# Performance work log

Measured on AMD Instinct MI355X. Metric: run time of the kernel, lower is better.

The kernel has to match this reference:

```python
import jax, jax.numpy as jnp
import numpy as np

B, P, N, E, F, L = 64, 512, 512, 128, 512, 6
SQRT_E = 11.313708498984761
CLIP = 10.0
EPS = 1e-5

def _inorm(x, w, b):
    # InstanceNorm1d over node dim (axis=1) per (batch, channel); x: [B,N,E]
    mu = x.mean(axis=1, keepdims=True)
    var = x.var(axis=1, keepdims=True)
    return (x - mu) * jax.lax.rsqrt(var + EPS) * w + b

def setup_inputs():
    key = jax.random.key(0)
    ks = jax.random.split(key, 24)
    nrm = lambda k, shp, s=0.05: jax.random.normal(k, shp, dtype=jnp.float32) * s
    inp = {}
    inp['data'] = jax.random.uniform(ks[0], (B, N, 2), dtype=jnp.float32)
    inp['dist'] = -jax.random.uniform(ks[1], (B, N, N), dtype=jnp.float32)      # negative dist
    inp['cur_dist'] = -jax.random.uniform(ks[2], (B, P, N), dtype=jnp.float32)
    inp['capacity'] = jax.random.uniform(ks[3], (B, P), dtype=jnp.float32)
    inp['ninf_mask'] = jnp.zeros((B, P, N), jnp.float32)
    inp['log_scale'] = jnp.array([1.0], jnp.float32)
    # encoder params (Linear weights stored [in,out], i.e. torch weight transposed)
    inp['emb_W'] = nrm(ks[4], (2, E), 0.5); inp['emb_b'] = jnp.zeros((E,), jnp.float32)
    inp['Wq'] = nrm(ks[5], (L, E, E)); inp['Wk'] = nrm(ks[6], (L, E, E)); inp['Wv'] = nrm(ks[7], (L, E, E))
    inp['aft_alpha'] = jnp.ones((L,), jnp.float32)
    inp['n1_w'] = jnp.ones((L, E), jnp.float32); inp['n1_b'] = jnp.zeros((L, E), jnp.float32)
    inp['ff_W1'] = nrm(ks[8], (L, E, F)); inp['ff_b1'] = jnp.zeros((L, F), jnp.float32)
    inp['ff_W2'] = nrm(ks[9], (L, F, E)); inp['ff_b2'] = jnp.zeros((L, E), jnp.float32)
    inp['n2_w'] = jnp.ones((L, E), jnp.float32); inp['n2_b'] = jnp.zeros((L, E), jnp.float32)
    # decoder params
    inp['dWq'] = nrm(ks[10], (E + 1, E)); inp['dWk'] = nrm(ks[11], (E, E)); inp['dWv'] = nrm(ks[12], (E, E))
    inp['dec_aft_alpha'] = jnp.array([1.0], jnp.float32)
    inp['probs_alpha'] = jnp.array([1.0], jnp.float32)
    return inp

def reference(data, dist, cur_dist, capacity, ninf_mask, log_scale,
              emb_W, emb_b, Wq, Wk, Wv, aft_alpha, n1_w, n1_b,
              ff_W1, ff_b1, ff_W2, ff_b2, n2_w, n2_b,
              dWq, dWk, dWv, dec_aft_alpha, probs_alpha):
    ls = log_scale[0]
    # ---- encoder: stacked AFT layers ----
    x = data @ emb_W + emb_b                                   # [B,N,E]
    for l in range(L):
        q = x @ Wq[l]; k = x @ Wk[l]; v = x @ Wv[l]
        ad = jnp.exp(ls * aft_alpha[l] * dist)                 # [B,N,N]
        ek = jnp.exp(k)
        weighted = (ad @ (ek * v)) / (ad @ ek)                 # [B,N,E]
        out = jax.nn.sigmoid(q) * weighted
        h = _inorm(x + out, n1_w[l], n1_b[l])
        ff = jax.nn.relu(h @ ff_W1[l] + ff_b1[l]) @ ff_W2[l] + ff_b2[l]
        x = _inorm(h + ff, n2_w[l], n2_b[l])
    enc = x                                                    # [B,N,E]
    # ---- decoder ----
    k = enc @ dWk; v = enc @ dWv
    gmean = enc.mean(axis=1, keepdims=True)                    # [B,1,E]
    gmp = jnp.broadcast_to(gmean, (enc.shape[0], capacity.shape[1], enc.shape[2]))
    q = jnp.concatenate([gmp, capacity[:, :, None]], axis=2) @ dWq   # [B,P,E]
    ad = jnp.exp(ls * dec_aft_alpha[0] * cur_dist + ninf_mask)       # [B,P,N]
    ek = jnp.exp(k)
    weighted = (ad @ (ek * v)) / (ad @ ek)                     # [B,P,E]
    aft = jax.nn.sigmoid(q) * weighted
    score = jnp.einsum('bpe,bne->bpn', aft, enc) / SQRT_E
    score = score + ls * probs_alpha[0] * cur_dist
    score = CLIP * jnp.tanh(score) + ninf_mask
    return jax.nn.softmax(score, axis=2)                       # [B,P,N]
```

## Files before the change

kernel.cpp:

```cpp
#include <hip/hip_runtime.h>
#include <math.h>

#define B_ 64
#define N_ 512
#define P_ 512
#define E_ 128
#define F_ 512
#define L_ 6
#define SQRT_E_INV 0.08838834764831843f

typedef unsigned short u16;
typedef __attribute__((ext_vector_type(8))) short bf8;
typedef __attribute__((ext_vector_type(16))) float f16v;

__device__ inline u16 bf16r(float f) {
    unsigned u = __float_as_uint(f);
    u += 0x7fffu + ((u >> 16) & 1u);
    return (u16)(u >> 16);
}
__device__ inline float bf2f(u16 h) { return __uint_as_float((unsigned)h << 16); }

#define MFMA(a, b, c) __builtin_amdgcn_mfma_f32_32x32x16_bf16(a, b, c, 0, 0, 0)

struct Q3 {
    const u16 *A0, *A1;
    const u16 *qh, *ql, *vh, *vl, *kh, *kl;
    u16 *sq16, *y2t;
};

__launch_bounds__(256, 2) __global__ void qvk3_k(Q3 p)
{
    const int tid = threadIdx.x;
    const int lane = tid & 63, wv = tid >> 6;
    const int wm = wv & 1, wn = wv >> 1;
    const int ln = lane & 31, hk = lane >> 5;
    const int row0 = blockIdx.x * 64;

    __shared__ __align__(16) u16 As[2][64][40];
    __shared__ __align__(16) u16 Bs[6][128][40];

    f16v aq[2], av[2], ak[2];
#pragma unroll
    for (int nt = 0; nt < 2; ++nt)
#pragma unroll
        for (int q = 0; q < 16; ++q) { aq[nt][q] = 0.f; av[nt][q] = 0.f; ak[nt][q] = 0.f; }

    const int r = tid >> 2, kq = tid & 3;
    for (int k0 = 0; k0 < 128; k0 += 32) {
        size_t ga = (size_t)(row0 + r) * 128 + k0 + kq * 8;
        *(uint4*)&As[0][r][kq * 8] = *(const uint4*)(p.A0 + ga);
        *(uint4*)&As[1][r][kq * 8] = *(const uint4*)(p.A1 + ga);
#pragma unroll
        for (int i = 0; i < 2; ++i) {
            int s = tid + i * 256;
            int rb2 = s >> 2, q = s & 3;
            size_t gb = (size_t)rb2 * 128 + k0 + q * 8;
            *(uint4*)&Bs[0][rb2][q * 8] = *(const uint4*)(p.qh + gb);
            *(uint4*)&Bs[1][rb2][q * 8] = *(const uint4*)(p.ql + gb);
            *(uint4*)&Bs[2][rb2][q * 8] = *(const uint4*)(p.vh + gb);
            *(uint4*)&Bs[3][rb2][q * 8] = *(const uint4*)(p.vl + gb);
            *(uint4*)&Bs[4][rb2][q * 8] = *(const uint4*)(p.kh + gb);
            *(uint4*)&Bs[5][rb2][q * 8] = *(const uint4*)(p.kl + gb);
        }
        __syncthreads();
#pragma unroll
        for (int s = 0; s < 2; ++s) {
            bf8 ah = *(const bf8*)&As[0][wm * 32 + ln][s * 16 + hk * 8];
            bf8 al = *(const bf8*)&As[1][wm * 32 + ln][s * 16 + hk * 8];
#pragma unroll
            for (int nt = 0; nt < 2; ++nt) {
                const int br = wn * 64 + nt * 32 + ln, sc = s * 16 + hk * 8;
                bf8 bqh = *(const bf8*)&Bs[0][br][sc];
                bf8 bql = *(const bf8*)&Bs[1][br][sc];
                bf8 bvh = *(const bf8*)&Bs[2][br][sc];
                bf8 bvl = *(const bf8*)&Bs[3][br][sc];
                bf8 bkh = *(const bf8*)&Bs[4][br][sc];
                bf8 bkl = *(const bf8*)&Bs[5][br][sc];
                aq[nt] = MFMA(ah, bqh, aq[nt]);
                aq[nt] = MFMA(ah, bql, aq[nt]);
                aq[nt] = MFMA(al, bqh, aq[nt]);
                av[nt] = MFMA(ah, bvh, av[nt]);
                av[nt] = MFMA(ah, bvl, av[nt]);
                av[nt] = MFMA(al, bvh, av[nt]);
                ak[nt] = MFMA(ah, bkh, ak[nt]);
// ... 5 lines not shown
    }

#pragma unroll
    for (int nt = 0; nt < 2; ++nt) {
        int gn = wn * 64 + nt * 32 + ln;
#pragma unroll
        for (int g = 0; g < 4; ++g) {
            int rb = row0 + wm * 32 + g * 8 + hk * 4;
            int bb = rb >> 9, nb = rb & 511;
            u16 pe[4], pv[4];
#pragma unroll
            for (int rr = 0; rr < 4; ++rr) {
                float vq = aq[nt][g * 4 + rr];
                p.sq16[(size_t)(rb + rr) * 128 + gn] =
                    bf16r(1.f / (1.f + __expf(-vq)));
                u16 hv = bf16r(av[nt][g * 4 + rr]);
                u16 he = bf16r(__expf(ak[nt][g * 4 + rr]));
                pe[rr] = he;
                pv[rr] = bf16r(bf2f(hv) * bf2f(he));
            }
            uint2 ue, uv;
            ue.x = pe[0] | ((unsigned)pe[1] << 16);
            ue.y = pe[2] | ((unsigned)pe[3] << 16);
            uv.x = pv[0] | ((unsigned)pv[1] << 16);
            uv.y = pv[2] | ((unsigned)pv[3] << 16);
            *(uint2*)(p.y2t + (size_t)bb * 131072 + (size_t)gn * 512 + nb) = uv;
            *(uint2*)(p.y2t + (size_t)bb * 131072 + (size_t)(128 + gn) * 512 + nb) = ue;
        }
    }
}

struct QV {
    const u16 *A0, *A1;
    const u16 *vh, *vl, *kh, *kl;
    u16* y2t;
};

__launch_bounds__(256, 3) __global__ void qvk_vk_k(QV p)
{
    const int tid = threadIdx.x;
    const int lane = tid & 63, wv = tid >> 6;
    const int wm = wv & 1, wn = wv >> 1;
    const int ln = lane & 31, hk = lane >> 5;
    const int row0 = blockIdx.x * 64;

    __shared__ __align__(16) u16 As[2][64][40];
    __shared__ __align__(16) u16 Bs[4][128][40];

    f16v av[2], ak[2];
#pragma unroll
    for (int nt = 0; nt < 2; ++nt)
#pragma unroll
        for (int q = 0; q < 16; ++q) { av[nt][q] = 0.f; ak[nt][q] = 0.f; }

    const int r = tid >> 2, kq = tid & 3;
    for (int k0 = 0; k0 < 128; k0 += 32) {
        size_t ga = (size_t)(row0 + r) * 128 + k0 + kq * 8;
        *(uint4*)&As[0][r][kq * 8] = *(const uint4*)(p.A0 + ga);
        *(uint4*)&As[1][r][kq * 8] = *(const uint4*)(p.A1 + ga);
#pragma unroll
        for (int i = 0; i < 2; ++i) {
            int s = tid + i * 256;
            int rb2 = s >> 2, q = s & 3;
            size_t gb = (size_t)rb2 * 128 + k0 + q * 8;
            *(uint4*)&Bs[0][rb2][q * 8] = *(const uint4*)(p.vh + gb);
            *(uint4*)&Bs[1][rb2][q * 8] = *(const uint4*)(p.vl + gb);
            *(uint4*)&Bs[2][rb2][q * 8] = *(const uint4*)(p.kh + gb);
            *(uint4*)&Bs[3][rb2][q * 8] = *(const uint4*)(p.kl + gb);
        }
        __syncthreads();
#pragma unroll
        for (int s = 0; s < 2; ++s) {
            bf8 ah = *(const bf8*)&As[0][wm * 32 + ln][s * 16 + hk * 8];
            bf8 al = *(const bf8*)&As[1][wm * 32 + ln][s * 16 + hk * 8];
#pragma unroll
            for (int nt = 0; nt < 2; ++nt) {
                const int br = wn * 64 + nt * 32 + ln, sc = s * 16 + hk * 8;
                bf8 bvh = *(const bf8*)&Bs[0][br][sc];
                bf8 bvl = *(const bf8*)&Bs[1][br][sc];
                bf8 bkh = *(const bf8*)&Bs[2][br][sc];
                bf8 bkl = *(const bf8*)&Bs[3][br][sc];
                av[nt] = MFMA(ah, bvh, av[nt]);
                av[nt] = MFMA(ah, bvl, av[nt]);
                av[nt] = MFMA(al, bvh, av[nt]);
                ak[nt] = MFMA(ah, bkh, ak[nt]);
                ak[nt] = MFMA(ah, bkl, ak[nt]);
                ak[nt] = MFMA(al, bkh, ak[nt]);
            }
        }
        __syncthreads();
    }

#pragma unroll
    for (int nt = 0; nt < 2; ++nt) {
        int gn = wn * 64 + nt * 32 + ln;
#pragma unroll
        for (int g = 0; g < 4; ++g) {
            int rb = row0 + wm * 32 + g * 8 + hk * 4;
            int bb = rb >> 9, nb = rb & 511;
            u16 pe[4], pv[4];
#pragma unroll
            for (int rr = 0; rr < 4; ++rr) {
                u16 hv = bf16r(av[nt][g * 4 + rr]);
                u16 he = bf16r(__expf(ak[nt][g * 4 + rr]));
                pe[rr] = he;
                pv[rr] = bf16r(bf2f(hv) * bf2f(he));
            }
            uint2 ue, uv;
            ue.x = pe[0] | ((unsigned)pe[1] << 16);
            ue.y = pe[2] | ((unsigned)pe[3] << 16);
            uv.x = pv[0] | ((unsigned)pv[1] << 16);
            uv.y = pv[2] | ((unsigned)pv[3] << 16);
            *(uint2*)(p.y2t + (size_t)bb * 131072 + (size_t)gn * 512 + nb) = uv;
            *(uint2*)(p.y2t + (size_t)bb * 131072 + (size_t)(128 + gn) * 512 + nb) = ue;
        }
    }
}

struct AP2 {
    const u16 *A16;
    const u16 *B0, *sq;
    u16 *gh, *gl;
    const float *s1, *s2; int s2i;
    const float *gq, *cap, *dWq;
};

template <int OPA, int SG>
__launch_bounds__(256, 3) __global__ void aft2_k(AP2 p)
{
    const int tid = threadIdx.x;
    const int lane = tid & 63, wv = tid >> 6;
    const int wm = wv & 1, wn = wv >> 1;
    const int ln = lane & 31, hk = lane >> 5;

    const int id = blockIdx.x;
    const int xcd = id & 7, slot = id >> 3;
    const int bz = xcd * 8 + (slot >> 3);
    const int row0 = (slot & 7) * 64;

    __shared__ __align__(16) u16 As[2][64][40];
    __shared__ __align__(16) u16 Bs[2][256][40];

    f16v acc[4];
#pragma unroll
    for (int j = 0; j < 4; ++j)
#pragma unroll
        for (int q = 0; q < 16; ++q) acc[j][q] = 0.f;

    const float ascale = (OPA == 1) ? p.s1[0] * p.s2[p.s2i] : 0.f;
    const u16* Af = p.A16 + (size_t)bz * 262144 + (size_t)row0 * 512;
    const u16* Bb = p.B0 + (size_t)bz * 131072;

    const int r = tid >> 2, kq = tid & 3;
    uint4 va;
    uint4 vb[4];

#define AFT_LOAD(K0)                                                          \
    {                                                                         \
        va = *(const uint4*)(Af + (size_t)r * 512 + (K0) + kq * 8);           \
        size_t gb = (size_t)tid * 512 + (K0);                                 \
// ... 21 lines not shown
            *(uint4*)&Bs[BUF][tid][q * 8] = vb[q];                            \
    }

#define AFT_COMPUTE(BUF)                                                      \
    {                                                                         \
        _Pragma("unroll") for (int s = 0; s < 2; ++s) {                       \
            bf8 ah = *(const bf8*)&As[BUF][wm * 32 + ln][s * 16 + hk * 8];    \
            _Pragma("unroll") for (int j = 0; j < 4; ++j) {                   \
                int br = ((j >> 1) << 7) + wn * 64 + ((j & 1) << 5) + ln;     \
                bf8 bh = *(const bf8*)&Bs[BUF][br][s * 16 + hk * 8];          \
                acc[j] = MFMA(ah, bh, acc[j]);                                \
            }                                                                 \
        }                                                                     \
    }

    AFT_LOAD(0);
    AFT_WRITE(0);
    __syncthreads();

    int cur = 0;
    for (int k0 = 32; k0 < 512; k0 += 32) {
        AFT_LOAD(k0);
        AFT_COMPUTE(cur);
        AFT_WRITE(cur ^ 1);
        __syncthreads();
        cur ^= 1;
    }
    AFT_COMPUTE(cur);

#undef AFT_LOAD
#undef AFT_WRITE
#undef AFT_COMPUTE

    const u16* sqb = (SG == 1) ? (p.sq + (size_t)bz * 65536) : (const u16*)0;
    u16* ghb = p.gh + (size_t)bz * 65536;
    u16* glb = p.gl + (size_t)bz * 65536;
#pragma unroll
    for (int j = 0; j < 2; ++j) {
        int e = wn * 64 + j * 32 + ln;
#pragma unroll
        for (int g = 0; g < 4; ++g) {
#pragma unroll
            for (int rr = 0; rr < 4; ++rr) {
                int row = row0 + wm * 32 + g * 8 + hk * 4 + rr;
                float num = acc[j][g * 4 + rr];
                float den = acc[j + 2][g * 4 + rr];
                float pv = num / den;
                if (SG == 1) pv *= bf2f(sqb[(size_t)row * 128 + e]);
                if (SG == 2) {
                    float qv = fmaf(p.cap[(size_t)bz * 512 + row],
                                    p.dWq[128 * 128 + e], p.gq[bz * 128 + e]);
                    pv *= 1.f / (1.f + __expf(-qv));
                }
                u16 hi = bf16r(pv);
                ghb[(size_t)row * 128 + e] = hi;
                glb[(size_t)row * 128 + e] = bf16r(pv - bf2f(hi));
            }
        }
    }
}

struct F12 {
    const u16 *A0, *A1;
    const u16 *w1h, *w1l;
    const u16 *w2h, *w2l;
    const float *b1, *b2;
    float* of;
};

__launch_bounds__(512, 2) __global__ void ffn12_k(F12 p)
{
    const int tid = threadIdx.x;
    const int lane = tid & 63, wv = tid >> 6;
    const int wm = wv & 1, wn = wv >> 1;
    const int ln = lane & 31, hk = lane >> 5;
    const int row0 = blockIdx.x * 64;

    __shared__ __align__(16) u16 Ws[2][2][128][72];
    __shared__ __align__(16) u16 ff1c[4][64][136];

    bf8 ar0[8], ar1[8];
    {
        const size_t arow = (size_t)(row0 + wm * 32 + ln) * 128;
#pragma unroll
        for (int s = 0; s < 8; ++s) {
            ar0[s] = *(const bf8*)(p.A0 + arow + s * 16 + hk * 8);
            ar1[s] = *(const bf8*)(p.A1 + arow + s * 16 + hk * 8);
        }
    }

    const int lcol = wn * 32 + ln;
    const int sc_ = tid >> 3, sq_ = tid & 7;
    uint4 wr[2][2];

#define F_LOAD1(CT, KC)                                                       \
    {                                                                         \
        _Pragma("unroll") for (int pl = 0; pl < 2; ++pl) {                    \
            const u16* src = pl ? p.w1l : p.w1h;                              \
            _Pragma("unroll") for (int it = 0; it < 2; ++it) {                \
                int c = sc_ + it * 64;                                        \
                wr[pl][it] = *(const uint4*)(src +                            \
                    (size_t)((CT) * 128 + c) * 128 + (KC) * 64 + sq_ * 8);    \
            }                                                                 \
        }                                                                     \
    }

#define F_LOAD2(J)                                                            \
    {                                                                         \
        _Pragma("unroll") for (int pl = 0; pl < 2; ++pl) {                    \
            const u16* src = pl ? p.w2l : p.w2h;                              \
            _Pragma("unroll") for (int it = 0; it < 2; ++it) {                \
                int c = sc_ + it * 64;                                        \
                wr[pl][it] = *(const uint4*)(src +                            \
                    (size_t)c * 512 + (J) * 64 + sq_ * 8);                    \
            }                                                                 \
        }                                                                     \
    }

#define F_STORE(BUF)                                                          \
    {                                                                         \
// ... 36 lines not shown
                }
        }
        F_STORE(buf ^ 1);
        __syncthreads();
        buf ^= 1;
    }

    f16v c0, c1;
#pragma unroll
    for (int q = 0; q < 16; ++q) { c0[q] = 0.f; c1[q] = 0.f; }
#pragma unroll
    for (int j = 0; j < 8; ++j) {
        if (j < 7) F_LOAD2(j + 1);
#pragma unroll
        for (int s = 0; s < 4; ++s) {
            bf8 af = *(const bf8*)&ff1c[j >> 1][wm * 32 + ln]
                                      [(j & 1) * 64 + s * 16 + hk * 8];
            bf8 bh = *(const bf8*)&Ws[buf][0][lcol][s * 16 + hk * 8];
            bf8 bl = *(const bf8*)&Ws[buf][1][lcol][s * 16 + hk * 8];
            c0 = MFMA(af, bh, c0);
            c1 = MFMA(af, bl, c1);
        }
        if (j < 7) {
            F_STORE(buf ^ 1);
            __syncthreads();
            buf ^= 1;
        }
    }

#undef F_LOAD1
#undef F_LOAD2
#undef F_STORE

    float bv = p.b2[lcol];
#pragma unroll
    for (int g = 0; g < 4; ++g)
#pragma unroll
        for (int rr = 0; rr < 4; ++rr) {
            int rb = row0 + wm * 32 + g * 8 + hk * 4 + rr;
            p.of[(size_t)rb * 128 + lcol] = c0[g * 4 + rr] + c1[g * 4 + rr] + bv;
        }
}

struct SP2 {
    const u16 *A0, *A1, *B0, *B1;
    float* out;
    const float *cd, *cm;
    const float *s1, *s2;
};

__launch_bounds__(1024, 4) __global__ void score_sm_k(SP2 p)
{
    const int tid = threadIdx.x;
    const int lane = tid & 63, wv = tid >> 6;
    const int wm = wv & 1, wn = wv >> 1;
    const int ln = lane & 31, hk = lane >> 5;

    const int id = blockIdx.x;
    const int xcd = id & 7, s_ = id >> 3;
    const int bz = xcd * 8 + (s_ & 7);
    const int row0 = (s_ >> 3) * 64;

    __shared__ __align__(16) u16 As[2][64][136];
    __shared__ __align__(16) u16 Bs[2][512][40];
    __shared__ float rs[8][64];

#pragma unroll
    for (int i = 0; i < 2; ++i) {
        int idx = tid + i * 1024;
        int pl = idx >> 10, rem = idx & 1023;
        int row = rem >> 4, q = rem & 15;
        const u16* src = pl ? p.A1 : p.A0;
        *(uint4*)&As[pl][row][q * 8] =
            *(const uint4*)(src + ((size_t)bz * 512 + row0 + row) * 128 + q * 8);
    }

    const float sp = p.s1[0] * p.s2[0];

    f16v accs[2];
#pragma unroll
    for (int nt = 0; nt < 2; ++nt)
#pragma unroll
        for (int q = 0; q < 16; ++q) accs[nt][q] = 0.f;

    for (int k0 = 0; k0 < 128; k0 += 32) {
#pragma unroll
        for (int i = 0; i < 4; ++i) {
            int idx = tid + i * 1024;
            int pl = idx >> 11, rem = idx & 2047;
            int row = rem >> 2, q = rem & 3;
            const u16* src = pl ? p.B1 : p.B0;
            *(uint4*)&Bs[pl][row][q * 8] =
                *(const uint4*)(src + ((size_t)bz * 512 + row) * 128 + k0 + q * 8);
        }
        __syncthreads();
#pragma unroll
        for (int s = 0; s < 2; ++s) {
            bf8 ah = *(const bf8*)&As[0][wm * 32 + ln][k0 + s * 16 + hk * 8];
            bf8 al = *(const bf8*)&As[1][wm * 32 + ln][k0 + s * 16 + hk * 8];
#pragma unroll
            for (int nt = 0; nt < 2; ++nt) {
                bf8 bh = *(const bf8*)&Bs[0][wn * 64 + nt * 32 + ln][s * 16 + hk * 8];
                bf8 bl = *(const bf8*)&Bs[1][wn * 64 + nt * 32 + ln][s * 16 + hk * 8];
                accs[nt] = MFMA(ah, bh, accs[nt]);
                accs[nt] = MFMA(ah, bl, accs[nt]);
                accs[nt] = MFMA(al, bh, accs[nt]);
            }
        }
        __syncthreads();
    }

    float rsum[16];
#pragma unroll
    for (int nt = 0; nt < 2; ++nt) {
        const int gn = wn * 64 + nt * 32 + ln;
        float cdv[16], cmv[16];
#pragma unroll
        for (int g = 0; g < 4; ++g)
#pragma unroll
            for (int rr = 0; rr < 4; ++rr) {
                int grow = row0 + wm * 32 + g * 8 + hk * 4 + rr;
                size_t ix = (size_t)bz * 262144 + (size_t)grow * 512 + gn;
                cdv[g * 4 + rr] = p.cd[ix];
                cmv[g * 4 + rr] = p.cm[ix];
            }
#pragma unroll
// ... 11 lines not shown
    for (int i = 0; i < 16; ++i) {
#pragma unroll
        for (int o = 1; o < 32; o <<= 1) rsum[i] += __shfl_xor(rsum[i], o);
    }
    __syncthreads();
    if (ln == 0) {
#pragma unroll
        for (int i = 0; i < 16; ++i) {
            int lr = wm * 32 + (i >> 2) * 8 + hk * 4 + (i & 3);
            rs[wn][lr] = rsum[i];
        }
    }
    __syncthreads();
    float invr[16];
#pragma unroll
    for (int i = 0; i < 16; ++i) {
        int lr = wm * 32 + (i >> 2) * 8 + hk * 4 + (i & 3);
        float t = rs[0][lr] + rs[1][lr] + rs[2][lr] + rs[3][lr]
                + rs[4][lr] + rs[5][lr] + rs[6][lr] + rs[7][lr];
        invr[i] = 1.f / t;
    }

#pragma unroll
    for (int nt = 0; nt < 2; ++nt) {
        int gn = wn * 64 + nt * 32 + ln;
#pragma unroll
        for (int g = 0; g < 4; ++g)
#pragma unroll
            for (int rr = 0; rr < 4; ++rr) {
                int grow = row0 + wm * 32 + g * 8 + hk * 4 + rr;
                size_t ix = (size_t)bz * 262144 + (size_t)grow * 512 + gn;
                p.out[ix] = accs[nt][g * 4 + rr] * invr[g * 4 + rr];
            }
    }
}

template <int MODE>
__launch_bounds__(256) __global__ void inorm_k(
    const u16* __restrict__ ah, const u16* __restrict__ al,
    const u16* __restrict__ g0, const u16* __restrict__ g1,
    const float* __restrict__ f1,
    const float* __restrict__ nw, const float* __restrict__ nbv,
    u16* __restrict__ oh, u16* __restrict__ ol)
{
    const int bb = blockIdx.x, e0 = blockIdx.y * 16;
    const int tid = threadIdx.x, el = tid & 3, no = tid >> 2;
    const size_t base = (size_t)bb * N_ * E_ + e0 + el * 4;

    float4 vals[8];
    float s1x = 0, s1y = 0, s1z = 0, s1w = 0;
    float s2x = 0, s2y = 0, s2z = 0, s2w = 0;
#pragma unroll
    for (int i = 0; i < 8; ++i) {
        int n = no * 8 + i;
        size_t ad = base + (size_t)n * E_;
        uint2 h2 = *(const uint2*)(ah + ad);
        uint2 l2 = *(const uint2*)(al + ad);
        float x0 = bf2f((u16)h2.x) + bf2f((u16)l2.x);
        float x1 = bf2f((u16)(h2.x >> 16)) + bf2f((u16)(l2.x >> 16));
        float x2 = bf2f((u16)h2.y) + bf2f((u16)l2.y);
        float x3 = bf2f((u16)(h2.y >> 16)) + bf2f((u16)(l2.y >> 16));
        float4 v;
        if (MODE == 1) {
            uint2 a2 = *(const uint2*)(g0 + ad);
            uint2 b2 = *(const uint2*)(g1 + ad);
            v.x = x0 + bf2f((u16)a2.x) + bf2f((u16)b2.x);
            v.y = x1 + bf2f((u16)(a2.x >> 16)) + bf2f((u16)(b2.x >> 16));
            v.z = x2 + bf2f((u16)a2.y) + bf2f((u16)b2.y);
            v.w = x3 + bf2f((u16)(a2.y >> 16)) + bf2f((u16)(b2.y >> 16));
        } else {
            float4 ff = *(const float4*)(f1 + ad);
            v.x = x0 + ff.x; v.y = x1 + ff.y; v.z = x2 + ff.z; v.w = x3 + ff.w;
        }
        vals[i] = v;
        s1x += v.x; s1y += v.y; s1z += v.z; s1w += v.w;
        s2x = fmaf(v.x, v.x, s2x); s2y = fmaf(v.y, v.y, s2y);
        s2z = fmaf(v.z, v.z, s2z); s2w = fmaf(v.w, v.w, s2w);
    }

    __shared__ float4 r1[256], r2[256];
    r1[tid] = make_float4(s1x, s1y, s1z, s1w);
    r2[tid] = make_float4(s2x, s2y, s2z, s2w);
    __syncthreads();
    for (int s = 128; s >= 4; s >>= 1) {
        if (tid < s) {
            float4 u = r1[tid], w = r1[tid + s];
            r1[tid] = make_float4(u.x + w.x, u.y + w.y, u.z + w.z, u.w + w.w);
            float4 pq = r2[tid], q = r2[tid + s];
            r2[tid] = make_float4(pq.x + q.x, pq.y + q.y, pq.z + q.z, pq.w + q.w);
        }
        __syncthreads();
    }
    __shared__ float4 mu_s[4], rs_s[4];
    if (tid < 4) {
        float4 m = r1[tid], q = r2[tid];
        m.x *= (1.f / N_); m.y *= (1.f / N_); m.z *= (1.f / N_); m.w *= (1.f / N_);
        q.x *= (1.f / N_); q.y *= (1.f / N_); q.z *= (1.f / N_); q.w *= (1.f / N_);
        float4 rsq;
        rsq.x = rsqrtf(q.x - m.x * m.x + 1e-5f);
        rsq.y = rsqrtf(q.y - m.y * m.y + 1e-5f);
        rsq.z = rsqrtf(q.z - m.z * m.z + 1e-5f);
        rsq.w = rsqrtf(q.w - m.w * m.w + 1e-5f);
        mu_s[tid] = m; rs_s[tid] = rsq;
    }
    __syncthreads();
    float4 mu = mu_s[el], rsq = rs_s[el];
    float4 w4 = *(const float4*)(nw + e0 + el * 4);
    float4 b4 = *(const float4*)(nbv + e0 + el * 4);
#pragma unroll
    for (int i = 0; i < 8; ++i) {
        size_t ad = base + (size_t)(no * 8 + i) * E_;
        float4 v = vals[i];
        v.x = fmaf((v.x - mu.x) * rsq.x, w4.x, b4.x);
        v.y = fmaf((v.y - mu.y) * rsq.y, w4.y, b4.y);
        v.z = fmaf((v.z - mu.z) * rsq.z, w4.z, b4.z);
        v.w = fmaf((v.w - mu.w) * rsq.w, w4.w, b4.w);
        u16 h0 = bf16r(v.x), h1 = bf16r(v.y), h2v = bf16r(v.z), h3 = bf16r(v.w);
        u16 l0 = bf16r(v.x - bf2f(h0)), l1 = bf16r(v.y - bf2f(h1));
        u16 l2v = bf16r(v.z - bf2f(h2v)), l3 = bf16r(v.w - bf2f(h3));
        uint2 ph, pl;
        ph.x = h0 | ((unsigned)h1 << 16); ph.y = h2v | ((unsigned)h3 << 16);
        pl.x = l0 | ((unsigned)l1 << 16); pl.y = l2v | ((unsigned)l3 << 16);
        *(uint2*)(oh + ad) = ph;
        *(uint2*)(ol + ad) = pl;
    }
}

__global__ void wprep_k(const float* __restrict__ W, u16* __restrict__ Th,
                        u16* __restrict__ Tl, int K, int N)
{
    const int z = blockIdx.z;
    const float* Wz = W + (size_t)z * K * N;
    u16* Hh = Th + (size_t)z * K * N;
    u16* Hl = Tl + (size_t)z * K * N;
    __shared__ float t[32][33];
    const int j = threadIdx.x & 31, i0 = threadIdx.x >> 5;
    const int k0 = blockIdx.x * 32, n0 = blockIdx.y * 32;
    for (int i = i0; i < 32; i += 8)
        t[i][j] = Wz[(size_t)(k0 + i) * N + n0 + j];
    __syncthreads();
    for (int i = i0; i < 32; i += 8) {
        float v = t[j][i];
        u16 h = bf16r(v);
        u16 l = bf16r(v - bf2f(h));
        size_t o = (size_t)(n0 + i) * K + k0 + j;
        Hh[o] = h; Hl[o] = l;
    }
}

__global__ void distprep_k(const float* __restrict__ src, u16* __restrict__ dst)
{
    size_t i = ((size_t)blockIdx.x * 256 + threadIdx.x) * 8;
    float4 f0 = *(const float4*)(src + i);
    float4 f1 = *(const float4*)(src + i + 4);
    uint4 pk;
    pk.x = bf16r(f0.x) | ((unsigned)bf16r(f0.y) << 16);
    pk.y = bf16r(f0.z) | ((unsigned)bf16r(f0.w) << 16);
// ... 3 lines not shown
}

__global__ void decprep_k(const float* __restrict__ cd, const float* __restrict__ nf,
                          const float* __restrict__ s1, const float* __restrict__ s2,
                          u16* __restrict__ dst)
{
    const float da = s1[0] * s2[0];
    size_t i = ((size_t)blockIdx.x * 256 + threadIdx.x) * 8;
    float4 c0 = *(const float4*)(cd + i);
    float4 c1 = *(const float4*)(cd + i + 4);
    float4 m0 = *(const float4*)(nf + i);
    float4 m1 = *(const float4*)(nf + i + 4);
    uint4 pk;
    pk.x = bf16r(fmaf(da, c0.x, m0.x)) | ((unsigned)bf16r(fmaf(da, c0.y, m0.y)) << 16);
    pk.y = bf16r(fmaf(da, c0.z, m0.z)) | ((unsigned)bf16r(fmaf(da, c0.w, m0.w)) << 16);
    pk.z = bf16r(fmaf(da, c1.x, m1.x)) | ((unsigned)bf16r(fmaf(da, c1.y, m1.y)) << 16);
    pk.w = bf16r(fmaf(da, c1.z, m1.z)) | ((unsigned)bf16r(fmaf(da, c1.w, m1.w)) << 16);
    *(uint4*)(dst + i) = pk;
}

__global__ void embed_k(const float* __restrict__ data, const float* __restrict__ W,
                        const float* __restrict__ bias,
                        u16* __restrict__ xh, u16* __restrict__ xl)
{
    size_t idx = (size_t)blockIdx.x * 256 + threadIdx.x;
    int e = idx & 127;
    size_t bn = idx >> 7;
    float v = fmaf(data[bn * 2], W[e], fmaf(data[bn * 2 + 1], W[128 + e], bias[e]));
    u16 h = bf16r(v);
    xh[idx] = h;
    xl[idx] = bf16r(v - bf2f(h));
}

__launch_bounds__(512) __global__
void gq_k(const u16* __restrict__ xh, const u16* __restrict__ xl,
          const float* __restrict__ dWq, float* __restrict__ gq)
{
    int b = blockIdx.x;
    int tid = threadIdx.x;
    int e = tid & 127, qd = tid >> 7;
    float s = 0.f;
    for (int n = qd; n < N_; n += 4) {
        size_t ix = ((size_t)b * N_ + n) * E_ + e;
        s += bf2f(xh[ix]) + bf2f(xl[ix]);
    }
    __shared__ float part[512];
    __shared__ float gm[128];
    part[tid] = s;
    __syncthreads();
    if (tid < 128)
        gm[tid] = (part[tid] + part[tid + 128] + part[tid + 256] + part[tid + 384]) *
                  (1.f / N_);
    __syncthreads();
    if (tid < 128) {
        float acc = 0.f;
        for (int kk = 0; kk < 128; ++kk) acc = fmaf(gm[kk], dWq[kk * 128 + tid], acc);
        gq[b * 128 + tid] = acc;
    }
}

extern "C" void kernel_launch(void* const* d_in, const int* in_sizes, int n_in,
                              void* d_out, int out_size, void* d_ws, size_t ws_size,
                              hipStream_t stream)
{
    const float* data      = (const float*)d_in[0];
    const float* dist      = (const float*)d_in[1];
    const float* cur_dist  = (const float*)d_in[2];
    const float* capacity  = (const float*)d_in[3];
    const float* ninf      = (const float*)d_in[4];
    const float* log_scale = (const float*)d_in[5];
    const float* emb_W     = (const float*)d_in[6];
    const float* emb_b     = (const float*)d_in[7];
    const float* Wq        = (const float*)d_in[8];
    const float* Wk        = (const float*)d_in[9];
    const float* Wv        = (const float*)d_in[10];
    const float* aft_alpha = (const float*)d_in[11];
    const float* n1_w      = (const float*)d_in[12];
    const float* n1_b      = (const float*)d_in[13];
    const float* ffW1      = (const float*)d_in[14];
    const float* ffb1      = (const float*)d_in[15];
    const float* ffW2      = (const float*)d_in[16];
    const float* ffb2      = (const float*)d_in[17];
    const float* n2_w      = (const float*)d_in[18];
    const float* n2_b      = (const float*)d_in[19];
    const float* dWq       = (const float*)d_in[20];
    const float* dWk       = (const float*)d_in[21];
    const float* dWv       = (const float*)d_in[22];
    const float* dec_alpha = (const float*)d_in[23];
    const float* p_alpha   = (const float*)d_in[24];
    float* out = (float*)d_out;

    char* W = (char*)d_ws;
    size_t off = 0;
    auto take = [&](size_t n) { void* pp = W + off; off += (n + 255) & ~(size_t)255; return pp; };
    const size_t SZP = (size_t)B_ * N_ * E_ * 2;

    u16* xh   = (u16*)take(SZP);
    u16* xl   = (u16*)take(SZP);
    u16* hh   = (u16*)take(SZP);
    u16* hl   = (u16*)take(SZP);
    u16* sq16 = (u16*)take(SZP);
    u16* gh   = (u16*)take(SZP);
    u16* gl   = (u16*)take(SZP);
    u16* y2t  = (u16*)take(2 * SZP);
    float* ff2 = (float*)take((size_t)B_ * N_ * E_ * 4);
    u16* d16  = (u16*)take((size_t)B_ * N_ * N_ * 2);
    u16* wqt_h = (u16*)take(196608); u16* wqt_l = (u16*)take(196608);
    u16* wkt_h = (u16*)take(196608); u16* wkt_l = (u16*)take(196608);
    u16* wvt_h = (u16*)take(196608); u16* wvt_l = (u16*)take(196608);
    u16* w1t_h = (u16*)take(786432); u16* w1t_l = (u16*)take(786432);
    u16* w2t_h = (u16*)take(786432); u16* w2t_l = (u16*)take(786432);
    u16* dkt_h = (u16*)take(32768);  u16* dkt_l = (u16*)take(32768);
    u16* dvt_h = (u16*)take(32768);  u16* dvt_l = (u16*)take(32768);
    float* gq = (float*)take(32768);
    if (ws_size < off) return;

    u16* am16 = d16;

    wprep_k<<<dim3(4, 4, 6), 256, 0, stream>>>(Wq, wqt_h, wqt_l, 128, 128);
    wprep_k<<<dim3(4, 4, 6), 256, 0, stream>>>(Wk, wkt_h, wkt_l, 128, 128);
    wprep_k<<<dim3(4, 4, 6), 256, 0, stream>>>(Wv, wvt_h, wvt_l, 128, 128);
    wprep_k<<<dim3(4, 16, 6), 256, 0, stream>>>(ffW1, w1t_h, w1t_l, 128, 512);
    wprep_k<<<dim3(16, 4, 6), 256, 0, stream>>>(ffW2, w2t_h, w2t_l, 512, 128);
    wprep_k<<<dim3(4, 4, 1), 256, 0, stream>>>(dWk, dkt_h, dkt_l, 128, 128);
    wprep_k<<<dim3(4, 4, 1), 256, 0, stream>>>(dWv, dvt_h, dvt_l, 128, 128);

    distprep_k<<<8192, 256, 0, stream>>>(dist, d16);
    embed_k<<<16384, 256, 0, stream>>>(data, emb_W, emb_b, xh, xl);

    for (int l = 0; l < L_; ++l) {
        Q3 q3{};
        q3.A0 = xh; q3.A1 = xl;
        q3.qh = wqt_h + l * 16384; q3.ql = wqt_l + l * 16384;
        q3.vh = wvt_h + l * 16384; q3.vl = wvt_l + l * 16384;
        q3.kh = wkt_h + l * 16384; q3.kl = wkt_l + l * 16384;
        q3.sq16 = sq16; q3.y2t = y2t;
        qvk3_k<<<512, 256, 0, stream>>>(q3);

        AP2 ap{};
        ap.A16 = d16; ap.B0 = y2t; ap.sq = sq16; ap.gh = gh; ap.gl = gl;
        ap.s1 = log_scale; ap.s2 = aft_alpha; ap.s2i = l;
        aft2_k<1, 1><<<512, 256, 0, stream>>>(ap);

        inorm_k<1><<<dim3(B_, 8), 256, 0, stream>>>(
            xh, xl, gh, gl, nullptr, n1_w + l * 128, n1_b + l * 128, hh, hl);

        F12 f12{};
        f12.A0 = hh; f12.A1 = hl;
        f12.w1h = w1t_h + l * 65536; f12.w1l = w1t_l + l * 65536;
        f12.w2h = w2t_h + l * 65536; f12.w2l = w2t_l + l * 65536;
        f12.b1 = ffb1 + l * 512; f12.b2 = ffb2 + l * 128;
        f12.of = ff2;
        ffn12_k<<<512, 512, 0, stream>>>(f12);

        inorm_k<2><<<dim3(B_, 8), 256, 0, stream>>>(
            hh, hl, nullptr, nullptr, ff2, n2_w + l * 128, n2_b + l * 128, xh, xl);
    }

    {
        QV qv{};
        qv.A0 = xh; qv.A1 = xl;
        qv.vh = dvt_h; qv.vl = dvt_l;
        qv.kh = dkt_h; qv.kl = dkt_l;
        qv.y2t = y2t;
        qvk_vk_k<<<512, 256, 0, stream>>>(qv);
        gq_k<<<B_, 512, 0, stream>>>(xh, xl, dWq, gq);

        decprep_k<<<8192, 256, 0, stream>>>(cur_dist, ninf, log_scale, dec_alpha, am16);

        AP2 ap{};
        ap.A16 = am16; ap.B0 = y2t; ap.gh = hh; ap.gl = hl;
        ap.s1 = log_scale; ap.s2 = dec_alpha; ap.s2i = 0;
        ap.gq = gq; ap.cap = capacity; ap.dWq = dWq;
        aft2_k<3, 2><<<512, 256, 0, stream>>>(ap);

        SP2 sp{};
        sp.A0 = hh; sp.A1 = hl; sp.B0 = xh; sp.B1 = xl;
        sp.out = out; sp.cd = cur_dist; sp.cm = ninf;
        sp.s1 = log_scale; sp.s2 = p_alpha;
        score_sm_k<<<512, 1024, 0, stream>>>(sp);
    }
}
```

Before: 1.055 ms.

## Fuse instance norms into neighbouring GEMM kernels via partial statistics

Removes the standalone inorm passes. The AFT and FFN kernels now add the residual in their epilogues, store the un-normalized sum as a bf16 hi/lo pair, and write per-64-row partial sums and sums of squares. Each consumer (qvk, ffn, score) rebuilds mean and rstd from those partials and applies the affine norm while loading its operands. The decoder's global-mean query is replaced by an algebraic shortcut: the node mean of the normalized encoder output equals the norm bias, so gq reduces to n2_b @ dWq. This cuts kernel launches and full-tensor read/write passes, at the cost of extra ALU work on loads and variance computed as E[x²]-mu², which is less numerically robust.

```diff
diff --git a/kernel.cpp b/kernel.cpp
--- a/kernel.cpp
+++ b/kernel.cpp
@@ -22,12 +22,30 @@
 
 #define MFMA(a, b, c) __builtin_amdgcn_mfma_f32_32x32x16_bf16(a, b, c, 0, 0, 0)
 
+__device__ inline void norm_coef(const float* ps, const float* w, const float* b,
+                                 int bz, int tid, float* muw, float* bb)
+{
+    if (tid < 128) {
+        const float* base = ps + (size_t)bz * 2048 + tid * 2;
+        float s = 0.f, q = 0.f;
+#pragma unroll
+        for (int k = 0; k < 8; ++k) { s += base[k * 256]; q += base[k * 256 + 1]; }
+        float mu = s * (1.f / 512.f);
+        float rs = rsqrtf(q * (1.f / 512.f) - mu * mu + 1e-5f);
+        float mw = rs * w[tid];
+        muw[tid] = mw;
+        bb[tid] = b[tid] - mu * mw;
+    }
+}
+
 struct Q3 {
     const u16 *A0, *A1;
+    const float *ps2, *pw, *pb;
     const u16 *qh, *ql, *vh, *vl, *kh, *kl;
     u16 *sq16, *y2t;
 };
 
+template <int NORM>
 __launch_bounds__(256, 2) __global__ void qvk3_k(Q3 p)
 {
     const int tid = threadIdx.x;
@@ -38,6 +56,10 @@
 
     __shared__ __align__(16) u16 As[2][64][40];
     __shared__ __align__(16) u16 Bs[6][128][40];
+    __shared__ float muw[128], bbv[128];
+
+    if (NORM) norm_coef(p.ps2, p.pw, p.pb, blockIdx.x >> 3, tid, muw, bbv);
+    __syncthreads();
 
     f16v aq[2], av[2], ak[2];
 #pragma unroll
@@ -48,8 +70,25 @@
     const int r = tid >> 2, kq = tid & 3;
     for (int k0 = 0; k0 < 128; k0 += 32) {
         size_t ga = (size_t)(row0 + r) * 128 + k0 + kq * 8;
-        *(uint4*)&As[0][r][kq * 8] = *(const uint4*)(p.A0 + ga);
-        *(uint4*)&As[1][r][kq * 8] = *(const uint4*)(p.A1 + ga);
+        uint4 h4 = *(const uint4*)(p.A0 + ga);
+        uint4 l4 = *(const uint4*)(p.A1 + ga);
+        if (NORM) {
+            u16 h8[8], l8[8], ho[8], lo8[8];
+            *(uint4*)h8 = h4; *(uint4*)l8 = l4;
+            const int e0 = k0 + kq * 8;
+#pragma unroll
+            for (int j2 = 0; j2 < 8; ++j2) {
+                float v = bf2f(h8[j2]) + bf2f(l8[j2]);
+                float x = fmaf(v, muw[e0 + j2], bbv[e0 + j2]);
+                u16 hi = bf16r(x);
+                ho[j2] = hi; lo8[j2] = bf16r(x - bf2f(hi));
+            }
+            *(uint4*)&As[0][r][kq * 8] = *(uint4*)ho;
+            *(uint4*)&As[1][r][kq * 8] = *(uint4*)lo8;
+        } else {
+            *(uint4*)&As[0][r][kq * 8] = h4;
+            *(uint4*)&As[1][r][kq * 8] = l4;
+        }
 #pragma unroll
         for (int i = 0; i < 2; ++i) {
             int s = tid + i * 256;
@@ -121,6 +160,7 @@
 
 struct QV {
     const u16 *A0, *A1;
+    const float *ps2, *pw, *pb;
     const u16 *vh, *vl, *kh, *kl;
     u16* y2t;
 };
@@ -135,6 +175,10 @@
 
     __shared__ __align__(16) u16 As[2][64][40];
     __shared__ __align__(16) u16 Bs[4][128][40];
+    __shared__ float muw[128], bbv[128];
+
+    norm_coef(p.ps2, p.pw, p.pb, blockIdx.x >> 3, tid, muw, bbv);
+    __syncthreads();
 
     f16v av[2], ak[2];
 #pragma unroll
@@ -145,8 +189,22 @@
     const int r = tid >> 2, kq = tid & 3;
     for (int k0 = 0; k0 < 128; k0 += 32) {
         size_t ga = (size_t)(row0 + r) * 128 + k0 + kq * 8;
-        *(uint4*)&As[0][r][kq * 8] = *(const uint4*)(p.A0 + ga);
-        *(uint4*)&As[1][r][kq * 8] = *(const uint4*)(p.A1 + ga);
+        uint4 h4 = *(const uint4*)(p.A0 + ga);
+        uint4 l4 = *(const uint4*)(p.A1 + ga);
+        {
+            u16 h8[8], l8[8], ho[8], lo8[8];
+            *(uint4*)h8 = h4; *(uint4*)l8 = l4;
+            const int e0 = k0 + kq * 8;
+#pragma unroll
+            for (int j2 = 0; j2 < 8; ++j2) {
+                float v = bf2f(h8[j2]) + bf2f(l8[j2]);
+                float x = fmaf(v, muw[e0 + j2], bbv[e0 + j2]);
+                u16 hi = bf16r(x);
+                ho[j2] = hi; lo8[j2] = bf16r(x - bf2f(hi));
+            }
+            *(uint4*)&As[0][r][kq * 8] = *(uint4*)ho;
+            *(uint4*)&As[1][r][kq * 8] = *(uint4*)lo8;
+        }
 #pragma unroll
         for (int i = 0; i < 2; ++i) {
             int s = tid + i * 256;
@@ -209,12 +267,15 @@
 struct AP2 {
     const u16 *A16;
     const u16 *B0, *sq;
+    const u16 *X0, *X1;
+    const float *ps2, *pw, *pb;
     u16 *gh, *gl;
+    float *ps1;
     const float *s1, *s2; int s2i;
-    const float *gq, *cap, *dWq;
+    const float *gq1, *cap, *dWq;
 };
 
-template <int OPA, int SG>
+template <int OPA, int SG, int RES, int NORM>
 __launch_bounds__(256, 3) __global__ void aft2_k(AP2 p)
 {
     const int tid = threadIdx.x;
@@ -302,12 +363,22 @@
 #undef AFT_WRITE
 #undef AFT_COMPUTE
 
+    __syncthreads();
+    float* fl = (float*)&As[0][0][0];
+    float* muw = fl;
+    float* bbv = fl + 128;
+    float* red = fl + 256;
+    if (RES && NORM) norm_coef(p.ps2, p.pw, p.pb, bz, tid, muw, bbv);
+    __syncthreads();
+
+    const int rslot = wm * 2 + hk;
     const u16* sqb = (SG == 1) ? (p.sq + (size_t)bz * 65536) : (const u16*)0;
     u16* ghb = p.gh + (size_t)bz * 65536;
     u16* glb = p.gl + (size_t)bz * 65536;
 #pragma unroll
     for (int j = 0; j < 2; ++j) {
         int e = wn * 64 + j * 32 + ln;
+        float ssum = 0.f, sq2 = 0.f;
 #pragma unroll
         for (int g = 0; g < 4; ++g) {
 #pragma unroll
@@ -319,23 +390,54 @@
                 if (SG == 1) pv *= bf2f(sqb[(size_t)row * 128 + e]);
                 if (SG == 2) {
                     float qv = fmaf(p.cap[(size_t)bz * 512 + row],
-                                    p.dWq[128 * 128 + e], p.gq[bz * 128 + e]);
+                                    p.dWq[128 * 128 + e], p.gq1[e]);
                     pv *= 1.f / (1.f + __expf(-qv));
                 }
-                u16 hi = bf16r(pv);
+                float outv = pv;
+                if (RES) {
+                    size_t xa = (size_t)bz * 65536 + (size_t)row * 128 + e;
+                    float xv = bf2f(p.X0[xa]) + bf2f(p.X1[xa]);
+                    if (NORM) xv = fmaf(xv, muw[e], bbv[e]);
+                    outv = xv + pv;
+                }
+                u16 hi = bf16r(outv);
+                u16 lo = bf16r(outv - bf2f(hi));
                 ghb[(size_t)row * 128 + e] = hi;
-                glb[(size_t)row * 128 + e] = bf16r(pv - bf2f(hi));
-            }
+                glb[(size_t)row * 128 + e] = lo;
+                if (RES) {
+                    float vr = bf2f(hi) + bf2f(lo);
+                    ssum += vr;
+                    sq2 = fmaf(vr, vr, sq2);
+                }
+            }
+        }
+        if (RES) {
+            red[rslot * 256 + e * 2] = ssum;
+            red[rslot * 256 + e * 2 + 1] = sq2;
+        }
+    }
+    if (RES) {
+        __syncthreads();
+        if (tid < 128) {
+            float s = red[tid * 2] + red[256 + tid * 2] +
+                      red[512 + tid * 2] + red[768 + tid * 2];
+            float q = red[tid * 2 + 1] + red[256 + tid * 2 + 1] +
+                      red[512 + tid * 2 + 1] + red[768 + tid * 2 + 1];
+            size_t po = ((size_t)bz * 8 + (row0 >> 6)) * 256 + tid * 2;
+            p.ps1[po] = s;
+            p.ps1[po + 1] = q;
         }
     }
 }
 
 struct F12 {
-    const u16 *A0, *A1;
+    const u16 *V0, *V1;
+    const float *ps1, *n1w, *n1b;
     const u16 *w1h, *w1l;
     const u16 *w2h, *w2l;
     const float *b1, *b2;
-    float* of;
+    u16 *o0, *o1;
+    float *ps2;
 };
 
 __launch_bounds__(512, 2) __global__ void ffn12_k(F12 p)
@@ -345,17 +447,34 @@
     const int wm = wv & 1, wn = wv >> 1;
     const int ln = lane & 31, hk = lane >> 5;
     const int row0 = blockIdx.x * 64;
+    const int b = blockIdx.x >> 3;
 
     __shared__ __align__(16) u16 Ws[2][2][128][72];
     __shared__ __align__(16) u16 ff1c[4][64][136];
+    __shared__ float muw1[128], bb1[128];
+
+    norm_coef(p.ps1, p.n1w, p.n1b, b, tid, muw1, bb1);
+    __syncthreads();
 
     bf8 ar0[8], ar1[8];
     {
         const size_t arow = (size_t)(row0 + wm * 32 + ln) * 128;
 #pragma unroll
         for (int s = 0; s < 8; ++s) {
-            ar0[s] = *(const bf8*)(p.A0 + arow + s * 16 + hk * 8);
-            ar1[s] = *(const bf8*)(p.A1 + arow + s * 16 + hk * 8);
+            uint4 h4 = *(const uint4*)(p.V0 + arow + s * 16 + hk * 8);
+            uint4 l4 = *(const uint4*)(p.V1 + arow + s * 16 + hk * 8);
+            u16 h8[8], l8[8], ho[8], lo8[8];
+            *(uint4*)h8 = h4; *(uint4*)l8 = l4;
+            const int e0 = s * 16 + hk * 8;
+#pragma unroll
+            for (int j2 = 0; j2 < 8; ++j2) {
+                float v = bf2f(h8[j2]) + bf2f(l8[j2]);
+                float h = fmaf(v, muw1[e0 + j2], bb1[e0 + j2]);
+                u16 hi = bf16r(h);
+                ho[j2] = hi; lo8[j2] = bf16r(h - bf2f(hi));
+            }
+            ar0[s] = *(bf8*)ho;
+            ar1[s] = *(bf8*)lo8;
         }
     }
 
@@ -458,18 +577,45 @@
 #undef F_LOAD2
 #undef F_STORE
 
-    float bv = p.b2[lcol];
+    const float bv = p.b2[lcol];
+    const float mwl = muw1[lcol], bbl = bb1[lcol];
+    float ssum = 0.f, sq2 = 0.f;
 #pragma unroll
     for (int g = 0; g < 4; ++g)
 #pragma unroll
         for (int rr = 0; rr < 4; ++rr) {
             int rb = row0 + wm * 32 + g * 8 + hk * 4 + rr;
-            p.of[(size_t)rb * 128 + lcol] = c0[g * 4 + rr] + c1[g * 4 + rr] + bv;
-        }
+            size_t xa = (size_t)rb * 128 + lcol;
+            float v1 = bf2f(p.V0[xa]) + bf2f(p.V1[xa]);
+            float h = fmaf(v1, mwl, bbl);
+            float val2 = h + c0[g * 4 + rr] + c1[g * 4 + rr] + bv;
+            u16 hi = bf16r(val2);
+            u16 lo = bf16r(val2 - bf2f(hi));
+            p.o0[xa] = hi;
+            p.o1[xa] = lo;
+            float vr = bf2f(hi) + bf2f(lo);
+            ssum += vr;
+            sq2 = fmaf(vr, vr, sq2);
+        }
+    __syncthreads();
+    float* red = (float*)&ff1c[0][0][0];
+    red[(wm * 2 + hk) * 256 + lcol * 2] = ssum;
+    red[(wm * 2 + hk) * 256 + lcol * 2 + 1] = sq2;
+    __syncthreads();
+    if (tid < 128) {
+        float s = red[tid * 2] + red[256 + tid * 2] +
+                  red[512 + tid * 2] + red[768 + tid * 2];
+        float q = red[tid * 2 + 1] + red[256 + tid * 2 + 1] +
+                  red[512 + tid * 2 + 1] + red[768 + tid * 2 + 1];
+        size_t po = ((size_t)b * 8 + (blockIdx.x & 7)) * 256 + tid * 2;
+        p.ps2[po] = s;
+        p.ps2[po + 1] = q;
+    }
 }
 
 struct SP2 {
     const u16 *A0, *A1, *B0, *B1;
+    const float *ps2, *pw, *pb;
     float* out;
     const float *cd, *cm;
     const float *s1, *s2;
@@ -490,6 +636,9 @@
     __shared__ __align__(16) u16 As[2][64][136];
     __shared__ __align__(16) u16 Bs[2][512][40];
     __shared__ float rs[8][64];
+    __shared__ float muw2[128], bb2[128];
+
+    norm_coef(p.ps2, p.pw, p.pb, bz, tid, muw2, bb2);
 
 #pragma unroll
     for (int i = 0; i < 2; ++i) {
@@ -500,6 +649,7 @@
         *(uint4*)&As[pl][row][q * 8] =
             *(const uint4*)(src + ((size_t)bz * 512 + row0 + row) * 128 + q * 8);
     }
+    __syncthreads();
 
     const float sp = p.s1[0] * p.s2[0];
 
@@ -511,13 +661,24 @@
 
     for (int k0 = 0; k0 < 128; k0 += 32) {
 #pragma unroll
-        for (int i = 0; i < 4; ++i) {
+        for (int i = 0; i < 2; ++i) {
             int idx = tid + i * 1024;
-            int pl = idx >> 11, rem = idx & 2047;
-            int row = rem >> 2, q = rem & 3;
-            const u16* src = pl ? p.B1 : p.B0;
-            *(uint4*)&Bs[pl][row][q * 8] =
-                *(const uint4*)(src + ((size_t)bz * 512 + row) * 128 + k0 + q * 8);
+            int row = idx >> 2, q = idx & 3;
+            size_t ga = ((size_t)bz * 512 + row) * 128 + k0 + q * 8;
+            uint4 h4 = *(const uint4*)(p.B0 + ga);
+            uint4 l4 = *(const uint4*)(p.B1 + ga);
+            u16 h8[8], l8[8], ho[8], lo8[8];
+            *(uint4*)h8 = h4; *(uint4*)l8 = l4;
+            const int e0 = k0 + q * 8;
+#pragma unroll
+            for (int j2 = 0; j2 < 8; ++j2) {
+                float v = bf2f(h8[j2]) + bf2f(l8[j2]);
+                float x = fmaf(v, muw2[e0 + j2], bb2[e0 + j2]);
+                u16 hi = bf16r(x);
+                ho[j2] = hi; lo8[j2] = bf16r(x - bf2f(hi));
+            }
+            *(uint4*)&Bs[0][row][q * 8] = *(uint4*)ho;
+            *(uint4*)&Bs[1][row][q * 8] = *(uint4*)lo8;
         }
         __syncthreads();
 #pragma unroll
@@ -595,97 +756,6 @@
                 size_t ix = (size_t)bz * 262144 + (size_t)grow * 512 + gn;
                 p.out[ix] = accs[nt][g * 4 + rr] * invr[g * 4 + rr];
             }
-    }
-}
-
-template <int MODE>
-__launch_bounds__(256) __global__ void inorm_k(
-    const u16* __restrict__ ah, const u16* __restrict__ al,
-    const u16* __restrict__ g0, const u16* __restrict__ g1,
-    const float* __restrict__ f1,
-    const float* __restrict__ nw, const float* __restrict__ nbv,
-    u16* __restrict__ oh, u16* __restrict__ ol)
-{
-    const int bb = blockIdx.x, e0 = blockIdx.y * 16;
-    const int tid = threadIdx.x, el = tid & 3, no = tid >> 2;
-    const size_t base = (size_t)bb * N_ * E_ + e0 + el * 4;
-
-    float4 vals[8];
-    float s1x = 0, s1y = 0, s1z = 0, s1w = 0;
-    float s2x = 0, s2y = 0, s2z = 0, s2w = 0;
-#pragma unroll
-    for (int i = 0; i < 8; ++i) {
-        int n = no * 8 + i;
-        size_t ad = base + (size_t)n * E_;
-        uint2 h2 = *(const uint2*)(ah + ad);
-        uint2 l2 = *(const uint2*)(al + ad);
-        float x0 = bf2f((u16)h2.x) + bf2f((u16)l2.x);
-        float x1 = bf2f((u16)(h2.x >> 16)) + bf2f((u16)(l2.x >> 16));
-        float x2 = bf2f((u16)h2.y) + bf2f((u16)l2.y);
-        float x3 = bf2f((u16)(h2.y >> 16)) + bf2f((u16)(l2.y >> 16));
-        float4 v;
-        if (MODE == 1) {
-            uint2 a2 = *(const uint2*)(g0 + ad);
-            uint2 b2 = *(const uint2*)(g1 + ad);
-            v.x = x0 + bf2f((u16)a2.x) + bf2f((u16)b2.x);
-            v.y = x1 + bf2f((u16)(a2.x >> 16)) + bf2f((u16)(b2.x >> 16));
-            v.z = x2 + bf2f((u16)a2.y) + bf2f((u16)b2.y);
-            v.w = x3 + bf2f((u16)(a2.y >> 16)) + bf2f((u16)(b2.y >> 16));
-        } else {
-            float4 ff = *(const float4*)(f1 + ad);
-            v.x = x0 + ff.x; v.y = x1 + ff.y; v.z = x2 + ff.z; v.w = x3 + ff.w;
-        }
-        vals[i] = v;
-        s1x += v.x; s1y += v.y; s1z += v.z; s1w += v.w;
-        s2x = fmaf(v.x, v.x, s2x); s2y = fmaf(v.y, v.y, s2y);
-        s2z = fmaf(v.z, v.z, s2z); s2w = fmaf(v.w, v.w, s2w);
-    }
-
-    __shared__ float4 r1[256], r2[256];
-    r1[tid] = make_float4(s1x, s1y, s1z, s1w);
-    r2[tid] = make_float4(s2x, s2y, s2z, s2w);
-    __syncthreads();
-    for (int s = 128; s >= 4; s >>= 1) {
-        if (tid < s) {
-            float4 u = r1[tid], w = r1[tid + s];
-            r1[tid] = make_float4(u.x + w.x, u.y + w.y, u.z + w.z, u.w + w.w);
-            float4 pq = r2[tid], q = r2[tid + s];
-            r2[tid] = make_float4(pq.x + q.x, pq.y + q.y, pq.z + q.z, pq.w + q.w);
-        }
-        __syncthreads();
-    }
-    __shared__ float4 mu_s[4], rs_s[4];
-    if (tid < 4) {
-        float4 m = r1[tid], q = r2[tid];
-        m.x *= (1.f / N_); m.y *= (1.f / N_); m.z *= (1.f / N_); m.w *= (1.f / N_);
-        q.x *= (1.f / N_); q.y *= (1.f / N_); q.z *= (1.f / N_); q.w *= (1.f / N_);
-        float4 rsq;
-        rsq.x = rsqrtf(q.x - m.x * m.x + 1e-5f);
-        rsq.y = rsqrtf(q.y - m.y * m.y + 1e-5f);
-        rsq.z = rsqrtf(q.z - m.z * m.z + 1e-5f);
-        rsq.w = rsqrtf(q.w - m.w * m.w + 1e-5f);
-        mu_s[tid] = m; rs_s[tid] = rsq;
-    }
-    __syncthreads();
-    float4 mu = mu_s[el], rsq = rs_s[el];
-    float4 w4 = *(const float4*)(nw + e0 + el * 4);
-    float4 b4 = *(const float4*)(nbv + e0 + el * 4);
-#pragma unroll
-    for (int i = 0; i < 8; ++i) {
-        size_t ad = base + (size_t)(no * 8 + i) * E_;
-        float4 v = vals[i];
-        v.x = fmaf((v.x - mu.x) * rsq.x, w4.x, b4.x);
-        v.y = fmaf((v.y - mu.y) * rsq.y, w4.y, b4.y);
-        v.z = fmaf((v.z - mu.z) * rsq.z, w4.z, b4.z);
-        v.w = fmaf((v.w - mu.w) * rsq.w, w4.w, b4.w);
-        u16 h0 = bf16r(v.x), h1 = bf16r(v.y), h2v = bf16r(v.z), h3 = bf16r(v.w);
-        u16 l0 = bf16r(v.x - bf2f(h0)), l1 = bf16r(v.y - bf2f(h1));
-        u16 l2v = bf16r(v.z - bf2f(h2v)), l3 = bf16r(v.w - bf2f(h3));
-        uint2 ph, pl;
-        ph.x = h0 | ((unsigned)h1 << 16); ph.y = h2v | ((unsigned)h3 << 16);
-        pl.x = l0 | ((unsigned)l1 << 16); pl.y = l2v | ((unsigned)l3 << 16);
-        *(uint2*)(oh + ad) = ph;
-        *(uint2*)(ol + ad) = pl;
     }
 }
 
@@ -755,31 +825,13 @@
     xl[idx] = bf16r(v - bf2f(h));
 }
 
-__launch_bounds__(512) __global__
-void gq_k(const u16* __restrict__ xh, const u16* __restrict__ xl,
-          const float* __restrict__ dWq, float* __restrict__ gq)
-{
-    int b = blockIdx.x;
-    int tid = threadIdx.x;
-    int e = tid & 127, qd = tid >> 7;
-    float s = 0.f;
-    for (int n = qd; n < N_; n += 4) {
-        size_t ix = ((size_t)b * N_ + n) * E_ + e;
-        s += bf2f(xh[ix]) + bf2f(xl[ix]);
-    }
-    __shared__ float part[512];
-    __shared__ float gm[128];
-    part[tid] = s;
-    __syncthreads();
-    if (tid < 128)
-        gm[tid] = (part[tid] + part[tid + 128] + part[tid + 256] + part[tid + 384]) *
-                  (1.f / N_);
-    __syncthreads();
-    if (tid < 128) {
-        float acc = 0.f;
-        for (int kk = 0; kk < 128; ++kk) acc = fmaf(gm[kk], dWq[kk * 128 + tid], acc);
-        gq[b * 128 + tid] = acc;
-    }
+__global__ void gqprep_k(const float* __restrict__ n2b,
+                         const float* __restrict__ dWq, float* __restrict__ gq1)
+{
+    int o = threadIdx.x;
+    float acc = 0.f;
+    for (int e = 0; e < 128; ++e) acc = fmaf(n2b[e], dWq[e * 128 + o], acc);
+    gq1[o] = acc;
 }
 
 extern "C" void kernel_launch(void* const* d_in, const int* in_sizes, int n_in,
@@ -823,11 +875,14 @@
     u16* hh   = (u16*)take(SZP);
     u16* hl   = (u16*)take(SZP);
     u16* sq16 = (u16*)take(SZP);
-    u16* gh   = (u16*)take(SZP);
-    u16* gl   = (u16*)take(SZP);
+    u16* vh1  = (u16*)take(SZP);
+    u16* vl1  = (u16*)take(SZP);
+    u16* vh2  = (u16*)take(SZP);
+    u16* vl2  = (u16*)take(SZP);
     u16* y2t  = (u16*)take(2 * SZP);
-    float* ff2 = (float*)take((size_t)B_ * N_ * E_ * 4);
     u16* d16  = (u16*)take((size_t)B_ * N_ * N_ * 2);
+    float* ps1 = (float*)take(64 * 8 * 128 * 2 * 4);
+    float* ps2 = (float*)take(64 * 8 * 128 * 2 * 4);
     u16* wqt_h = (u16*)take(196608); u16* wqt_l = (u16*)take(196608);
     u16* wkt_h = (u16*)take(196608); u16* wkt_l = (u16*)take(196608);
     u16* wvt_h = (u16*)take(196608); u16* wvt_l = (u16*)take(196608);
@@ -835,7 +890,7 @@
     u16* w2t_h = (u16*)take(786432); u16* w2t_l = (u16*)take(786432);
     u16* dkt_h = (u16*)take(32768);  u16* dkt_l = (u16*)take(32768);
     u16* dvt_h = (u16*)take(32768);  u16* dvt_l = (u16*)take(32768);
-    float* gq = (float*)take(32768);
+    float* gq1 = (float*)take(512);
     if (ws_size < off) return;
 
     u16* am16 = d16;
@@ -852,53 +907,65 @@
     embed_k<<<16384, 256, 0, stream>>>(data, emb_W, emb_b, xh, xl);
 
     for (int l = 0; l < L_; ++l) {
+        const u16* cxh = l ? vh2 : xh;
+        const u16* cxl = l ? vl2 : xl;
+        const float* ppw = l ? (n2_w + (l - 1) * 128) : n2_w;
+        const float* ppb = l ? (n2_b + (l - 1) * 128) : n2_b;
+
         Q3 q3{};
-        q3.A0 = xh; q3.A1 = xl;
+        q3.A0 = cxh; q3.A1 = cxl;
+        q3.ps2 = ps2; q3.pw = ppw; q3.pb = ppb;
         q3.qh = wqt_h + l * 16384; q3.ql = wqt_l + l * 16384;
         q3.vh = wvt_h + l * 16384; q3.vl = wvt_l + l * 16384;
         q3.kh = wkt_h + l * 16384; q3.kl = wkt_l + l * 16384;
         q3.sq16 = sq16; q3.y2t = y2t;
-        qvk3_k<<<512, 256, 0, stream>>>(q3);
+        if (l == 0) qvk3_k<0><<<512, 256, 0, stream>>>(q3);
+        else        qvk3_k<1><<<512, 256, 0, stream>>>(q3);
 
         AP2 ap{};
-        ap.A16 = d16; ap.B0 = y2t; ap.sq = sq16; ap.gh = gh; ap.gl = gl;
+        ap.A16 = d16; ap.B0 = y2t; ap.sq = sq16;
+        ap.X0 = cxh; ap.X1 = cxl;
+        ap.ps2 = ps2; ap.pw = ppw; ap.pb = ppb;
+        ap.gh = vh1; ap.gl = vl1; ap.ps1 = ps1;
         ap.s1 = log_scale; ap.s2 = aft_alpha; ap.s2i = l;
-        aft2_k<1, 1><<<512, 256, 0, stream>>>(ap);
-
-        inorm_k<1><<<dim3(B_, 8), 256, 0, stream>>>(
-            xh, xl, gh, gl, nullptr, n1_w + l * 128, n1_b + l * 128, hh, hl);
+        if (l == 0) aft2_k<1, 1, 1, 0><<<512, 256, 0, stream>>>(ap);
+        else        aft2_k<1, 1, 1, 1><<<512, 256, 0, stream>>>(ap);
 
         F12 f12{};
-        f12.A0 = hh; f12.A1 = hl;
+        f12.V0 = vh1; f12.V1 = vl1;
+        f12.ps1 = ps1; f12.n1w = n1_w + l * 128; f12.n1b = n1_b + l * 128;
         f12.w1h = w1t_h + l * 65536; f12.w1l = w1t_l + l * 65536;
         f12.w2h = w2t_h + l * 65536; f12.w2l = w2t_l + l * 65536;
         f12.b1 = ffb1 + l * 512; f12.b2 = ffb2 + l * 128;
-        f12.of = ff2;
+        f12.o0 = vh2; f12.o1 = vl2; f12.ps2 = ps2;
         ffn12_k<<<512, 512, 0, stream>>>(f12);
-
-        inorm_k<2><<<dim3(B_, 8), 256, 0, stream>>>(
-            hh, hl, nullptr, nullptr, ff2, n2_w + l * 128, n2_b + l * 128, xh, xl);
     }
 
     {
+        const float* lw = n2_w + (L_ - 1) * 128;
+        const float* lb = n2_b + (L_ - 1) * 128;
+
         QV qv{};
-        qv.A0 = xh; qv.A1 = xl;
+        qv.A0 = vh2; qv.A1 = vl2;
+        qv.ps2 = ps2; qv.pw = lw; qv.pb = lb;
         qv.vh = dvt_h; qv.vl = dvt_l;
         qv.kh = dkt_h; qv.kl = dkt_l;
         qv.y2t = y2t;
         qvk_vk_k<<<512, 256, 0, stream>>>(qv);
-        gq_k<<<B_, 512, 0, stream>>>(xh, xl, dWq, gq);
-
+
+        gqprep_k<<<1, 128, 0, stream>>>(lb, dWq, gq1);
         decprep_k<<<8192, 256, 0, stream>>>(cur_dist, ninf, log_scale, dec_alpha, am16);
 
         AP2 ap{};
-        ap.A16 = am16; ap.B0 = y2t; ap.gh = hh; ap.gl = hl;
+        ap.A16 = am16; ap.B0 = y2t;
+        ap.gh = hh; ap.gl = hl;
         ap.s1 = log_scale; ap.s2 = dec_alpha; ap.s2i = 0;
-        ap.gq = gq; ap.cap = capacity; ap.dWq = dWq;
-        aft2_k<3, 2><<<512, 256, 0, stream>>>(ap);
+        ap.gq1 = gq1; ap.cap = capacity; ap.dWq = dWq;
+        aft2_k<3, 2, 0, 0><<<512, 256, 0, stream>>>(ap);
 
         SP2 sp{};
-        sp.A0 = hh; sp.A1 = hl; sp.B0 = xh; sp.B1 = xl;
+        sp.A0 = hh; sp.A1 = hl; sp.B0 = vh2; sp.B1 = vl2;
+        sp.ps2 = ps2; sp.pw = lw; sp.pb = lb;
         sp.out = out; sp.cd = cur_dist; sp.cm = ninf;
         sp.s1 = log_scale; sp.s2 = p_alpha;
         score_sm_k<<<512, 1024, 0, stream>>>(sp);
```

After: 989.2 us. 6.3% less time.
